# Kernel tuning notes

Hardware: AMD Instinct MI355X
Metric: run time of the kernel (lower is better)

Reference implementation:

```python
import jax, jax.numpy as jnp
import numpy as np

DIM = 128

def setup_inputs() -> dict:
    key = jax.random.key(0)
    ks = jax.random.split(key, 5)
    B, N, C = 4096, 64, DIM
    x = jax.random.normal(ks[0], (B, N, C), dtype=jnp.float32)
    w_qkv = jax.random.normal(ks[1], (C, 3 * C), dtype=jnp.float32) / np.sqrt(C)
    b_qkv = jax.random.normal(ks[2], (3 * C,), dtype=jnp.float32) * 0.01
    w_proj = jax.random.normal(ks[3], (C, C), dtype=jnp.float32) / np.sqrt(C)
    b_proj = jax.random.normal(ks[4], (C,), dtype=jnp.float32) * 0.01
    return {"x": x, "w_qkv": w_qkv, "b_qkv": b_qkv, "w_proj": w_proj, "b_proj": b_proj}

def reference(x, w_qkv, b_qkv, w_proj, b_proj):
    B, N, C = x.shape
    qkv = x @ w_qkv + b_qkv                      # [B,N,3C]
    q, k, v = jnp.split(qkv, 3, axis=-1)         # each [B,N,C]
    attn = jnp.einsum('bnc,bmc->bnm', q, k) * (C ** -0.5)
    attn = jax.nn.softmax(attn, axis=-1)
    out = jnp.einsum('bnm,bmc->bnc', attn, v)
    return out @ w_proj + b_proj
```

## Files before the change

### kernel.cpp

```cpp
#include <hip/hip_runtime.h>

using bf16x8 = __attribute__((ext_vector_type(8))) short;
using f32x4  = __attribute__((ext_vector_type(4))) float;

__device__ __forceinline__ unsigned short f2bf(float f) {
  unsigned u = __builtin_bit_cast(unsigned, f);
  u += 0x7fffu + ((u >> 16) & 1u);
  return (unsigned short)(u >> 16);
}

__global__ void prep_weights(const float* __restrict__ wqkv,
                             const float* __restrict__ wproj,
                             unsigned short* __restrict__ ws) {
  int idx = blockIdx.x * 256 + threadIdx.x;
  if (idx < 49152) {
    int c = idx >> 7, k = idx & 127;
    ws[idx] = f2bf(wqkv[k * 384 + c]);
  } else {
    int i = idx - 49152;
    int c = i >> 7, k = i & 127;
    ws[49152 + i] = f2bf(wproj[k * 128 + c]);
  }
}

__global__ __launch_bounds__(256) void win_attn(
    const float* __restrict__ x, const float* __restrict__ bqkv,
    const float* __restrict__ bproj, const unsigned short* __restrict__ ws,
    float* __restrict__ out) {
  __shared__ unsigned short sA[9216];
  __shared__ unsigned short sB[8704];
  __shared__ unsigned short sC[8704];

  const int tid  = threadIdx.x;
  const int wave = tid >> 6;
  const int lane = tid & 63;
  const int g    = lane >> 4;
  const int lr   = lane & 15;
  const int b    = blockIdx.x;
  const float* xb = x + (size_t)b * 8192;

  #pragma unroll
  for (int i = 0; i < 8; ++i) {
    int e = tid + 256 * i;
    float4 v = ((const float4*)xb)[e];
    int flat = e << 2;
    int r = flat >> 7, c = flat & 127;
    ushort4 pk = make_ushort4(f2bf(v.x), f2bf(v.y), f2bf(v.z), f2bf(v.w));
    *(ushort4*)&sA[r * 136 + c] = pk;
  }
  __syncthreads();

  f32x4 acc[4][6];
  #pragma unroll
  for (int rt = 0; rt < 4; ++rt)
    #pragma unroll
    for (int ct = 0; ct < 6; ++ct)
      acc[rt][ct] = f32x4{0.f, 0.f, 0.f, 0.f};

  float bias[6];
  #pragma unroll
  for (int ct = 0; ct < 6; ++ct) bias[ct] = bqkv[96 * wave + 16 * ct + lr];

  #pragma unroll
  for (int k0 = 0; k0 < 128; k0 += 32) {
    bf16x8 a[4];
    #pragma unroll
    for (int rt = 0; rt < 4; ++rt)
      a[rt] = *(const bf16x8*)&sA[(16 * rt + lr) * 136 + k0 + 8 * g];
    #pragma unroll
    for (int ct = 0; ct < 6; ++ct) {
      bf16x8 bf = *(const bf16x8*)&ws[(96 * wave + 16 * ct + lr) * 128 + k0 + 8 * g];
      #pragma unroll
      for (int rt = 0; rt < 4; ++rt)
        acc[rt][ct] = __builtin_amdgcn_mfma_f32_16x16x32_bf16(a[rt], bf, acc[rt][ct], 0, 0, 0);
    }
  }
  __syncthreads();

  #pragma unroll
  for (int rt = 0; rt < 4; ++rt) {
    #pragma unroll
    for (int ct = 0; ct < 6; ++ct) {
      int c  = 96 * wave + 16 * ct + lr;
      int r0 = 16 * rt + 4 * g;
      f32x4 v = acc[rt][ct];
      float bb = bias[ct];
      if (c < 128) {
        #pragma unroll
        for (int j = 0; j < 4; ++j) sB[(r0 + j) * 136 + c] = f2bf(v[j] + bb);
      } else if (c < 256) {
        #pragma unroll
        for (int j = 0; j < 4; ++j) sC[(r0 + j) * 136 + (c - 128)] = f2bf(v[j] + bb);
      } else {
        ushort4 pk = make_ushort4(f2bf(v[0] + bb), f2bf(v[1] + bb),
                                  f2bf(v[2] + bb), f2bf(v[3] + bb));
        *(ushort4*)&sA[(c - 256) * 72 + r0] = pk;
      }
    }
  }
  __syncthreads();

  f32x4 s[4];
  #pragma unroll
  for (int ct = 0; ct < 4; ++ct) s[ct] = f32x4{0.f, 0.f, 0.f, 0.f};
  #pragma unroll
  for (int k0 = 0; k0 < 128; k0 += 32) {
    bf16x8 a = *(const bf16x8*)&sB[(16 * wave + lr) * 136 + k0 + 8 * g];
    #pragma unroll
    for (int ct = 0; ct < 4; ++ct) {
      bf16x8 bf = *(const bf16x8*)&sC[(16 * ct + lr) * 136 + k0 + 8 * g];
      s[ct] = __builtin_amdgcn_mfma_f32_16x16x32_bf16(a, bf, s[ct], 0, 0, 0);
    }
  }
  __syncthreads();

  const float scale = 0.08838834764831845f;
  const float l2e   = 1.4426950408889634f;
  float rs[4];
  #pragma unroll
  for (int j = 0; j < 4; ++j) {
    float mm = fmaxf(fmaxf(s[0][j], s[1][j]), fmaxf(s[2][j], s[3][j])) * scale;
    #pragma unroll
    for (int off = 1; off < 16; off <<= 1) mm = fmaxf(mm, __shfl_xor(mm, off, 64));
    float ss = 0.f;
    #pragma unroll
    for (int ct = 0; ct < 4; ++ct) {
      float p = exp2f((s[ct][j] * scale - mm) * l2e);
      s[ct][j] = p;
      ss += p;
    }
    #pragma unroll
    for (int off = 1; off < 16; off <<= 1) ss += __shfl_xor(ss, off, 64);
    rs[j] = 1.0f / ss;
  }
  #pragma unroll
  for (int ct = 0; ct < 4; ++ct)
    #pragma unroll
    for (int j = 0; j < 4; ++j)
      sC[(16 * wave + 4 * g + j) * 72 + 16 * ct + lr] = f2bf(s[ct][j]);
  __syncthreads();

  f32x4 o[8];
  #pragma unroll
  for (int ct = 0; ct < 8; ++ct) o[ct] = f32x4{0.f, 0.f, 0.f, 0.f};
  #pragma unroll
  for (int k0 = 0; k0 < 64; k0 += 32) {
    bf16x8 a = *(const bf16x8*)&sC[(16 * wave + lr) * 72 + k0 + 8 * g];
    #pragma unroll
    for (int ct = 0; ct < 8; ++ct) {
      bf16x8 bf = *(const bf16x8*)&sA[(16 * ct + lr) * 72 + k0 + 8 * g];
      o[ct] = __builtin_amdgcn_mfma_f32_16x16x32_bf16(a, bf, o[ct], 0, 0, 0);
    }
  }
  #pragma unroll
  for (int ct = 0; ct < 8; ++ct)
    #pragma unroll
    for (int j = 0; j < 4; ++j)
      sB[(16 * wave + 4 * g + j) * 136 + 16 * ct + lr] = f2bf(o[ct][j] * rs[j]);
  __syncthreads();

  f32x4 y[8];
  #pragma unroll
  for (int ct = 0; ct < 8; ++ct) y[ct] = f32x4{0.f, 0.f, 0.f, 0.f};
  const unsigned short* wp = ws + 49152;
  #pragma unroll
  for (int k0 = 0; k0 < 128; k0 += 32) {
    bf16x8 a = *(const bf16x8*)&sB[(16 * wave + lr) * 136 + k0 + 8 * g];
    #pragma unroll
    for (int ct = 0; ct < 8; ++ct) {
      bf16x8 bf = *(const bf16x8*)&wp[(16 * ct + lr) * 128 + k0 + 8 * g];
      y[ct] = __builtin_amdgcn_mfma_f32_16x16x32_bf16(a, bf, y[ct], 0, 0, 0);
    }
  }
  float* ob = out + (size_t)b * 8192;
  #pragma unroll
  for (int ct = 0; ct < 8; ++ct) {
    float bb = bproj[16 * ct + lr];
    #pragma unroll
    for (int j = 0; j < 4; ++j) {
      int r = 16 * wave + 4 * g + j, c = 16 * ct + lr;
      ob[r * 128 + c] = y[ct][j] + bb;
    }
  }
}

extern "C" void kernel_launch(void* const* d_in, const int* in_sizes, int n_in,
                              void* d_out, int out_size, void* d_ws, size_t ws_size,
                              hipStream_t stream) {
  const float* x     = (const float*)d_in[0];
  const float* wqkv  = (const float*)d_in[1];
  const float* bqkv  = (const float*)d_in[2];
  const float* wproj = (const float*)d_in[3];
  const float* bproj = (const float*)d_in[4];
  float* out = (float*)d_out;
  unsigned short* ws = (unsigned short*)d_ws;

  prep_weights<<<256, 256, 0, stream>>>(wqkv, wproj, ws);
  win_attn<<<4096, 256, 0, stream>>>(x, bqkv, bproj, ws, out);
}
```

Before: 341.9 us.

## Fold Q·Kᵀ and V·Wproj weight products algebraically and reorder attention

Precomputes Wq·Wkᵀ and Wv·Wproj in the prep kernel, so attention scores become x·M·xᵀ, and the query bias is absorbed into a per-key softmax factor. The value/projection path becomes (P·diag(u))·(x·W2), normalised through an extra MFMA column. This drops the separate QKV projection and output projection GEMMs, cuts the main kernel's MFMA work, and lets it use less shared memory with an XOR swizzle and an occupancy hint of 4. The cost is more bf16 rounding from the folded weight products and exponentials, a heavier prep kernel, and accuracy that depends on how the bias terms are handled.

```diff
diff --git a/kernel.cpp b/kernel.cpp
--- a/kernel.cpp
+++ b/kernel.cpp
@@ -9,177 +9,206 @@
   return (unsigned short)(u >> 16);
 }
 
-__global__ void prep_weights(const float* __restrict__ wqkv,
-                             const float* __restrict__ wproj,
-                             unsigned short* __restrict__ ws) {
-  int idx = blockIdx.x * 256 + threadIdx.x;
-  if (idx < 49152) {
-    int c = idx >> 7, k = idx & 127;
-    ws[idx] = f2bf(wqkv[k * 384 + c]);
-  } else {
-    int i = idx - 49152;
-    int c = i >> 7, k = i & 127;
-    ws[49152 + i] = f2bf(wproj[k * 128 + c]);
-  }
-}
-
-__global__ __launch_bounds__(256) void win_attn(
-    const float* __restrict__ x, const float* __restrict__ bqkv,
-    const float* __restrict__ bproj, const unsigned short* __restrict__ ws,
+__global__ __launch_bounds__(128) void prep_weights(
+    const float* __restrict__ wqkv, const float* __restrict__ bqkv,
+    const float* __restrict__ wproj, const float* __restrict__ bproj,
+    void* __restrict__ ws) {
+  __shared__ float W[128][129];
+  unsigned short* wsu = (unsigned short*)ws;
+  float* wsF = (float*)ws;
+  const int tid = threadIdx.x;
+  const int cp = blockIdx.x & 127;
+  const bool second = blockIdx.x >= 128;
+  const int off = second ? 256 : 0;
+  for (int r = 0; r < 128; ++r)
+    W[r][tid] = wqkv[r * 384 + off + tid];
+  __syncthreads();
+  float acc = 0.f;
+  #pragma unroll 8
+  for (int o = 0; o < 128; ++o) {
+    float bc = second ? wproj[o * 128 + cp] : wqkv[cp * 384 + 128 + o];
+    acc += W[tid][o] * bc;
+  }
+  wsu[(second ? 16384 : 0) + cp * 128 + tid] = f2bf(acc);
+  if (tid == 0) {
+    float a2 = 0.f;
+    if (!second) {
+      for (int o = 0; o < 128; ++o) a2 += wqkv[cp * 384 + 128 + o] * bqkv[o];
+      wsF[16384 + cp] = a2;
+    } else {
+      for (int o = 0; o < 128; ++o) a2 += bqkv[256 + o] * wproj[o * 128 + cp];
+      wsF[16512 + cp] = a2 + bproj[cp];
+    }
+  }
+}
+
+__global__ __launch_bounds__(256, 4) void win_attn(
+    const float* __restrict__ x, const void* __restrict__ ws,
     float* __restrict__ out) {
-  __shared__ unsigned short sA[9216];
-  __shared__ unsigned short sB[8704];
-  __shared__ unsigned short sC[8704];
+  __shared__ unsigned short sX[8192];
+  __shared__ unsigned short sT[8192];
+  const unsigned short* MB  = (const unsigned short*)ws;
+  const unsigned short* W2B = MB + 16384;
+  const float* v2 = (const float*)((const char*)ws + 65536);
+  const float* b2 = v2 + 128;
 
   const int tid  = threadIdx.x;
   const int wave = tid >> 6;
   const int lane = tid & 63;
   const int g    = lane >> 4;
   const int lr   = lane & 15;
-  const int b    = blockIdx.x;
-  const float* xb = x + (size_t)b * 8192;
+  const float* xb = x + (size_t)blockIdx.x * 8192;
+  const float scale = 0.08838834764831845f;
+  const float l2e   = 1.4426950408889634f;
 
   #pragma unroll
   for (int i = 0; i < 8; ++i) {
     int e = tid + 256 * i;
     float4 v = ((const float4*)xb)[e];
-    int flat = e << 2;
-    int r = flat >> 7, c = flat & 127;
+    int r = e >> 5, c4 = (e & 31) * 4;
     ushort4 pk = make_ushort4(f2bf(v.x), f2bf(v.y), f2bf(v.z), f2bf(v.w));
-    *(ushort4*)&sA[r * 136 + c] = pk;
-  }
-  __syncthreads();
-
-  f32x4 acc[4][6];
-  #pragma unroll
-  for (int rt = 0; rt < 4; ++rt)
-    #pragma unroll
-    for (int ct = 0; ct < 6; ++ct)
-      acc[rt][ct] = f32x4{0.f, 0.f, 0.f, 0.f};
-
-  float bias[6];
-  #pragma unroll
-  for (int ct = 0; ct < 6; ++ct) bias[ct] = bqkv[96 * wave + 16 * ct + lr];
-
-  #pragma unroll
-  for (int k0 = 0; k0 < 128; k0 += 32) {
-    bf16x8 a[4];
-    #pragma unroll
-    for (int rt = 0; rt < 4; ++rt)
-      a[rt] = *(const bf16x8*)&sA[(16 * rt + lr) * 136 + k0 + 8 * g];
-    #pragma unroll
-    for (int ct = 0; ct < 6; ++ct) {
-      bf16x8 bf = *(const bf16x8*)&ws[(96 * wave + 16 * ct + lr) * 128 + k0 + 8 * g];
-      #pragma unroll
-      for (int rt = 0; rt < 4; ++rt)
-        acc[rt][ct] = __builtin_amdgcn_mfma_f32_16x16x32_bf16(a[rt], bf, acc[rt][ct], 0, 0, 0);
-    }
-  }
-  __syncthreads();
-
-  #pragma unroll
-  for (int rt = 0; rt < 4; ++rt) {
-    #pragma unroll
-    for (int ct = 0; ct < 6; ++ct) {
-      int c  = 96 * wave + 16 * ct + lr;
-      int r0 = 16 * rt + 4 * g;
-      f32x4 v = acc[rt][ct];
-      float bb = bias[ct];
-      if (c < 128) {
-        #pragma unroll
-        for (int j = 0; j < 4; ++j) sB[(r0 + j) * 136 + c] = f2bf(v[j] + bb);
-      } else if (c < 256) {
-        #pragma unroll
-        for (int j = 0; j < 4; ++j) sC[(r0 + j) * 136 + (c - 128)] = f2bf(v[j] + bb);
-      } else {
-        ushort4 pk = make_ushort4(f2bf(v[0] + bb), f2bf(v[1] + bb),
-                                  f2bf(v[2] + bb), f2bf(v[3] + bb));
-        *(ushort4*)&sA[(c - 256) * 72 + r0] = pk;
-      }
-    }
-  }
-  __syncthreads();
-
-  f32x4 s[4];
-  #pragma unroll
-  for (int ct = 0; ct < 4; ++ct) s[ct] = f32x4{0.f, 0.f, 0.f, 0.f};
-  #pragma unroll
-  for (int k0 = 0; k0 < 128; k0 += 32) {
-    bf16x8 a = *(const bf16x8*)&sB[(16 * wave + lr) * 136 + k0 + 8 * g];
-    #pragma unroll
-    for (int ct = 0; ct < 4; ++ct) {
-      bf16x8 bf = *(const bf16x8*)&sC[(16 * ct + lr) * 136 + k0 + 8 * g];
-      s[ct] = __builtin_amdgcn_mfma_f32_16x16x32_bf16(a, bf, s[ct], 0, 0, 0);
-    }
-  }
-  __syncthreads();
-
-  const float scale = 0.08838834764831845f;
-  const float l2e   = 1.4426950408889634f;
-  float rs[4];
-  #pragma unroll
-  for (int j = 0; j < 4; ++j) {
-    float mm = fmaxf(fmaxf(s[0][j], s[1][j]), fmaxf(s[2][j], s[3][j])) * scale;
-    #pragma unroll
-    for (int off = 1; off < 16; off <<= 1) mm = fmaxf(mm, __shfl_xor(mm, off, 64));
-    float ss = 0.f;
-    #pragma unroll
-    for (int ct = 0; ct < 4; ++ct) {
-      float p = exp2f((s[ct][j] * scale - mm) * l2e);
-      s[ct][j] = p;
-      ss += p;
-    }
-    #pragma unroll
-    for (int off = 1; off < 16; off <<= 1) ss += __shfl_xor(ss, off, 64);
-    rs[j] = 1.0f / ss;
-  }
-  #pragma unroll
-  for (int ct = 0; ct < 4; ++ct)
-    #pragma unroll
-    for (int j = 0; j < 4; ++j)
-      sC[(16 * wave + 4 * g + j) * 72 + 16 * ct + lr] = f2bf(s[ct][j]);
-  __syncthreads();
-
-  f32x4 o[8];
-  #pragma unroll
-  for (int ct = 0; ct < 8; ++ct) o[ct] = f32x4{0.f, 0.f, 0.f, 0.f};
-  #pragma unroll
-  for (int k0 = 0; k0 < 64; k0 += 32) {
-    bf16x8 a = *(const bf16x8*)&sC[(16 * wave + lr) * 72 + k0 + 8 * g];
-    #pragma unroll
-    for (int ct = 0; ct < 8; ++ct) {
-      bf16x8 bf = *(const bf16x8*)&sA[(16 * ct + lr) * 72 + k0 + 8 * g];
-      o[ct] = __builtin_amdgcn_mfma_f32_16x16x32_bf16(a, bf, o[ct], 0, 0, 0);
+    *(ushort4*)&sX[r * 128 + (c4 ^ ((r & 7) << 3))] = pk;
+  }
+  __syncthreads();
+
+  float wacc = 0.f;
+  {
+    const int r = 16 * wave + lr;
+    #pragma unroll
+    for (int ii = 0; ii < 4; ++ii) {
+      int c0 = 32 * g + 8 * ii;
+      bf16x8 f = *(const bf16x8*)&sX[r * 128 + (c0 ^ ((r & 7) << 3))];
+      #pragma unroll
+      for (int e2 = 0; e2 < 8; ++e2) {
+        float xf = __builtin_bit_cast(float, ((unsigned)(unsigned short)f[e2]) << 16);
+        wacc += xf * v2[c0 + e2];
+      }
+    }
+    wacc += __shfl_xor(wacc, 16, 64);
+    wacc += __shfl_xor(wacc, 32, 64);
+  }
+  const float uu = exp2f(wacc * (scale * l2e));
+
+  f32x4 accT[8];
+  #pragma unroll
+  for (int ct = 0; ct < 8; ++ct) accT[ct] = f32x4{0.f,0.f,0.f,0.f};
+  {
+    const int ra = 16 * wave + lr;
+    #pragma unroll
+    for (int k0 = 0; k0 < 128; k0 += 32) {
+      bf16x8 a = *(const bf16x8*)&sX[ra * 128 + ((k0 + 8 * g) ^ ((ra & 7) << 3))];
+      #pragma unroll
+      for (int ct = 0; ct < 8; ++ct) {
+        bf16x8 bv = *(const bf16x8*)&MB[(16 * ct + lr) * 128 + k0 + 8 * g];
+        accT[ct] = __builtin_amdgcn_mfma_f32_16x16x32_bf16(a, bv, accT[ct], 0, 0, 0);
+      }
     }
   }
   #pragma unroll
   for (int ct = 0; ct < 8; ++ct)
-    #pragma unroll
-    for (int j = 0; j < 4; ++j)
-      sB[(16 * wave + 4 * g + j) * 136 + 16 * ct + lr] = f2bf(o[ct][j] * rs[j]);
-  __syncthreads();
-
-  f32x4 y[8];
-  #pragma unroll
-  for (int ct = 0; ct < 8; ++ct) y[ct] = f32x4{0.f, 0.f, 0.f, 0.f};
-  const unsigned short* wp = ws + 49152;
-  #pragma unroll
-  for (int k0 = 0; k0 < 128; k0 += 32) {
-    bf16x8 a = *(const bf16x8*)&sB[(16 * wave + lr) * 136 + k0 + 8 * g];
-    #pragma unroll
-    for (int ct = 0; ct < 8; ++ct) {
-      bf16x8 bf = *(const bf16x8*)&wp[(16 * ct + lr) * 128 + k0 + 8 * g];
-      y[ct] = __builtin_amdgcn_mfma_f32_16x16x32_bf16(a, bf, y[ct], 0, 0, 0);
-    }
-  }
-  float* ob = out + (size_t)b * 8192;
-  #pragma unroll
-  for (int ct = 0; ct < 8; ++ct) {
-    float bb = bproj[16 * ct + lr];
     #pragma unroll
     for (int j = 0; j < 4; ++j) {
       int r = 16 * wave + 4 * g + j, c = 16 * ct + lr;
-      ob[r * 128 + c] = y[ct][j] + bb;
+      sT[r * 128 + (c ^ ((r & 7) << 3))] = f2bf(accT[ct][j]);
+    }
+
+  f32x4 s[4];
+  #pragma unroll
+  for (int ct = 0; ct < 4; ++ct) s[ct] = f32x4{0.f,0.f,0.f,0.f};
+  {
+    const int ra = 16 * wave + lr;
+    #pragma unroll
+    for (int k0 = 0; k0 < 128; k0 += 32) {
+      bf16x8 a = *(const bf16x8*)&sT[ra * 128 + ((k0 + 8 * g) ^ ((ra & 7) << 3))];
+      #pragma unroll
+      for (int ct = 0; ct < 4; ++ct) {
+        int rb = 16 * ct + lr;
+        bf16x8 bv = *(const bf16x8*)&sX[rb * 128 + ((k0 + 8 * g) ^ ((rb & 7) << 3))];
+        s[ct] = __builtin_amdgcn_mfma_f32_16x16x32_bf16(a, bv, s[ct], 0, 0, 0);
+      }
+    }
+  }
+  #pragma unroll
+  for (int j = 0; j < 4; ++j) {
+    float mm = fmaxf(fmaxf(s[0][j], s[1][j]), fmaxf(s[2][j], s[3][j]));
+    #pragma unroll
+    for (int off = 1; off < 16; off <<= 1) mm = fmaxf(mm, __shfl_xor(mm, off, 64));
+    const int r = 16 * wave + 4 * g + j;
+    #pragma unroll
+    for (int ct = 0; ct < 4; ++ct) {
+      float p = exp2f((s[ct][j] - mm) * (scale * l2e));
+      sT[r * 128 + ((16 * ct + lr) ^ ((r & 7) << 3))] = f2bf(p);
+    }
+  }
+
+  f32x4 z[8];
+  #pragma unroll
+  for (int ct = 0; ct < 8; ++ct) z[ct] = f32x4{0.f,0.f,0.f,0.f};
+  {
+    const int ra = 16 * wave + lr;
+    #pragma unroll
+    for (int k0 = 0; k0 < 128; k0 += 32) {
+      bf16x8 a = *(const bf16x8*)&sX[ra * 128 + ((k0 + 8 * g) ^ ((ra & 7) << 3))];
+      #pragma unroll
+      for (int ct = 0; ct < 8; ++ct) {
+        bf16x8 bv = *(const bf16x8*)&W2B[(16 * ct + lr) * 128 + k0 + 8 * g];
+        z[ct] = __builtin_amdgcn_mfma_f32_16x16x32_bf16(a, bv, z[ct], 0, 0, 0);
+      }
+    }
+  }
+  __syncthreads();
+
+  {
+    const int m0 = 16 * wave + 4 * g;
+    float u4[4];
+    #pragma unroll
+    for (int j = 0; j < 4; ++j) u4[j] = __shfl(uu, 4 * g + j, 64);
+    #pragma unroll
+    for (int ct = 0; ct < 8; ++ct) {
+      const int c = 16 * ct + lr;
+      ushort4 pk = make_ushort4(f2bf(z[ct][0] * u4[0]), f2bf(z[ct][1] * u4[1]),
+                                f2bf(z[ct][2] * u4[2]), f2bf(z[ct][3] * u4[3]));
+      if (ct < 4) *(ushort4*)&sT[c * 128 + 64 + (m0 ^ ((c & 7) << 3))] = pk;
+      else        *(ushort4*)&sX[(c - 64) * 128 + (m0 ^ ((c & 7) << 3))] = pk;
+    }
+    if (g == 0) sX[64 + 16 * wave + lr] = f2bf(uu);
+  }
+  __syncthreads();
+
+  f32x4 y[8], y8;
+  #pragma unroll
+  for (int ct = 0; ct < 8; ++ct) y[ct] = f32x4{0.f,0.f,0.f,0.f};
+  y8 = f32x4{0.f,0.f,0.f,0.f};
+  {
+    const int ra = 16 * wave + lr;
+    #pragma unroll
+    for (int k0 = 0; k0 < 64; k0 += 32) {
+      const int mk = k0 + 8 * g;
+      bf16x8 a = *(const bf16x8*)&sT[ra * 128 + (mk ^ ((ra & 7) << 3))];
+      #pragma unroll
+      for (int ct = 0; ct < 8; ++ct) {
+        const int c = 16 * ct + lr;
+        bf16x8 bv = (ct < 4)
+          ? *(const bf16x8*)&sT[c * 128 + 64 + (mk ^ ((c & 7) << 3))]
+          : *(const bf16x8*)&sX[(c - 64) * 128 + (mk ^ ((c & 7) << 3))];
+        y[ct] = __builtin_amdgcn_mfma_f32_16x16x32_bf16(a, bv, y[ct], 0, 0, 0);
+      }
+      bf16x8 uv = *(const bf16x8*)&sX[64 + mk];
+      y8 = __builtin_amdgcn_mfma_f32_16x16x32_bf16(a, uv, y8, 0, 0, 0);
+    }
+  }
+  float* ob = out + (size_t)blockIdx.x * 8192;
+  float rs4[4];
+  #pragma unroll
+  for (int j = 0; j < 4; ++j) rs4[j] = 1.0f / y8[j];
+  #pragma unroll
+  for (int ct = 0; ct < 8; ++ct) {
+    const int c = 16 * ct + lr;
+    const float bb = b2[c];
+    #pragma unroll
+    for (int j = 0; j < 4; ++j) {
+      int r = 16 * wave + 4 * g + j;
+      ob[r * 128 + c] = y[ct][j] * rs4[j] + bb;
     }
   }
 }
@@ -193,8 +222,7 @@
   const float* wproj = (const float*)d_in[3];
   const float* bproj = (const float*)d_in[4];
   float* out = (float*)d_out;
-  unsigned short* ws = (unsigned short*)d_ws;
-
-  prep_weights<<<256, 256, 0, stream>>>(wqkv, wproj, ws);
-  win_attn<<<4096, 256, 0, stream>>>(x, bqkv, bproj, ws, out);
-}
+
+  prep_weights<<<256, 128, 0, stream>>>(wqkv, bqkv, wproj, bproj, d_ws);
+  win_attn<<<4096, 256, 0, stream>>>(x, d_ws, out);
+}
```

After: 372.0 us. +8.8%, slower.
